# Kernel tuning notes

Measured on AMD Instinct MI355X. Metric: run time of the kernel, lower is better.

The kernel has to match this reference:

```python
import jax, jax.numpy as jnp
import numpy as np

N, E = 50000, 800000
C_IN, C_OUT, DIM, K = 64, 64, 3, 2
EPS = 1e-5


def setup_inputs() -> dict:
    key = jax.random.key(0)
    k1, k2, k3, k4, k5 = jax.random.split(key, 5)
    x = jax.random.normal(k1, (N, C_IN), dtype=jnp.float32)
    edge_index = jax.random.randint(k2, (2, E), 0, N, dtype=jnp.int32)
    edge_attr = jax.random.uniform(k3, (E, DIM), dtype=jnp.float32)  # pseudo coords in [0,1]
    W = jax.random.normal(k4, (K ** DIM, C_IN, C_OUT), dtype=jnp.float32) * 0.05
    root = jax.random.normal(k5, (C_IN, C_OUT), dtype=jnp.float32) * 0.05
    gamma = jnp.ones((C_OUT,), dtype=jnp.float32)
    beta = jnp.zeros((C_OUT,), dtype=jnp.float32)
    return {"x": x, "edge_attr": edge_attr, "W": W, "root": root,
            "gamma": gamma, "beta": beta, "edge_index": edge_index}


def _spline_basis(edge_attr):
    """Degree-1 open B-spline basis. Returns (weights [E,2^D], kernel idx [E,2^D])."""
    D = edge_attr.shape[1]
    v = edge_attr * (K - 1)                      # [E, D]
    k0 = jnp.floor(v)
    frac = v - k0                                # in [0,1)
    k0 = k0.astype(jnp.int32)
    bits = np.stack(np.unravel_index(np.arange(2 ** D), (2,) * D), axis=-1).astype(np.int32)  # [2^D, D]
    bits_f = jnp.asarray(bits, dtype=edge_attr.dtype)
    # per-dim weight: frac if bit else (1 - frac); product over dims
    w = jnp.where(bits_f[None] > 0, frac[:, None, :], 1.0 - frac[:, None, :])  # [E, 2^D, D]
    weights = jnp.prod(w, axis=-1)               # [E, 2^D]
    idx_d = jnp.clip(k0[:, None, :] + bits[None], 0, K - 1)  # [E, 2^D, D]
    radix = jnp.asarray(K ** np.arange(D), dtype=jnp.int32)
    idx = jnp.sum(idx_d * radix, axis=-1)        # [E, 2^D] in [0, K^D)
    return weights, idx


def reference(x, edge_attr, W, root, gamma, beta, edge_index):
    src, dst = edge_index[0], edge_index[1]
    Etot = edge_attr.shape[0]
    S = W.shape[0]  # K^D

    weights, idx = _spline_basis(edge_attr)      # [E, 2^D] each
    # dense per-edge basis over all K^D kernel slots
    B = jnp.zeros((Etot, S), dtype=x.dtype).at[jnp.arange(Etot)[:, None], idx].add(weights)

    xj = x[src]                                  # [E, C_in] gather
    z = (B[:, :, None] * xj[:, None, :]).reshape(Etot, S * x.shape[1])  # [E, S*C_in]
    msg = z @ W.reshape(S * x.shape[1], W.shape[2])                     # [E, C_out]

    agg = jax.ops.segment_sum(msg, dst, num_segments=x.shape[0])        # scatter-add
    cnt = jax.ops.segment_sum(jnp.ones((Etot,), dtype=x.dtype), dst, num_segments=x.shape[0])
    out = agg / jnp.maximum(cnt, 1.0)[:, None] + x @ root               # mean aggr + root weight

    # BatchNorm over nodes (training-mode batch stats)
    mean = jnp.mean(out, axis=0)
    var = jnp.var(out, axis=0)
    y = (out - mean) * jax.lax.rsqrt(var + EPS) * gamma + beta
    return jax.nn.elu(y)
```

## Files before the change

kernel.cpp:

```cpp
#include <hip/hip_runtime.h>
#include <hip/hip_bf16.h>
#include <cstdint>
#include <cstddef>

#define NN 50000
#define NE 800000
#define EPS 1e-5f
#define CAP 64

typedef short bf16x8 __attribute__((ext_vector_type(8)));
typedef float f32x4  __attribute__((ext_vector_type(4)));
typedef float f32x2  __attribute__((ext_vector_type(2)));


#define NB_WT   144
#define NB_MFMA 782
#define NB_SCAT 3125

static __device__ __forceinline__ ushort f2bf(float f) {
    __hip_bfloat16 h = __float2bfloat16(f);
    return *reinterpret_cast<ushort*>(&h);
}
static __device__ __forceinline__ float bf_lo(uint32_t u) {
    return __uint_as_float(u << 16);
}
static __device__ __forceinline__ float bf_hi(uint32_t u) {
    return __uint_as_float(u & 0xffff0000u);
}
static __device__ __forceinline__ uint32_t pack2(float a, float b) {
    return (uint32_t)f2bf(a) | ((uint32_t)f2bf(b) << 16);
}

__global__ __launch_bounds__(256) void wt_prep_k(const float* __restrict__ W,
                                                 const float* __restrict__ root,
                                                 ushort* __restrict__ WTg,
                                                 float* __restrict__ bnps,
                                                 float* __restrict__ bnpq) {
    const int idx = blockIdx.x * 256 + threadIdx.x;
    const int s  = idx >> 12;
    const int co = (idx >> 6) & 63;
    const int ci = idx & 63;
    const float v = (s < 8) ? W[s * 4096 + ci * 64 + co] : root[ci * 64 + co];
    WTg[idx] = f2bf(v);
    if (idx < 4096) { bnps[idx] = 0.f; bnpq[idx] = 0.f; }
}

__global__ __launch_bounds__(256) void fused_mfma_scatter_k(
        const float* __restrict__ x, const ushort* __restrict__ WTg,
        const int* __restrict__ ei, const float* __restrict__ attr,
        int* __restrict__ deg, int2* __restrict__ recs,
        uint8_t* __restrict__ H8, ushort* __restrict__ Hrootb) {
    __shared__ __align__(16) ushort XA[64 * 64];
    __shared__ __align__(16) ushort WT[64 * 64];
    const int t = threadIdx.x;
    const int b = blockIdx.x;

    if (b >= NB_MFMA) {
        const int e = (b - NB_MFMA) * 256 + t;
        if (e >= NE) return;
        const int src = ei[e];
        const int dst = ei[NE + e];
        const float f0 = attr[(size_t)e * 3 + 0];
        const float f1 = attr[(size_t)e * 3 + 1];
        const float f2 = attr[(size_t)e * 3 + 2];
        const uint32_t q = (uint32_t)rintf(f0 * 1023.f)
                         | ((uint32_t)rintf(f1 * 1023.f) << 10)
                         | ((uint32_t)rintf(f2 * 1023.f) << 20);
        const int p = atomicAdd(&deg[dst], 1);
        if (p < CAP) recs[(size_t)dst * CAP + p] = make_int2(src, (int)q);
        return;
    }

    const int n0 = b * 64;

    #pragma unroll
    for (int rep = 0; rep < 2; ++rep) {
        const int vt   = rep * 256 + t;
        const int row  = vt >> 3;
        const int col8 = vt & 7;
        const int n = n0 + row;
        uint4 u;
        if (n < NN) {
            const float4 v0 = *(const float4*)&x[(size_t)n * 64 + col8 * 8];
            const float4 v1 = *(const float4*)&x[(size_t)n * 64 + col8 * 8 + 4];
            u.x = pack2(v0.x, v0.y); u.y = pack2(v0.z, v0.w);
            u.z = pack2(v1.x, v1.y); u.w = pack2(v1.z, v1.w);
        } else {
            u = make_uint4(0, 0, 0, 0);
        }
        const int idx = (row * 64 + col8 * 8) ^ ((row & 7) << 3);
        *(uint4*)&XA[idx] = u;
    }

    const int w    = t >> 6;
    const int lane = t & 63;
    const int mrow = lane & 15;
    const int kgrp = lane >> 4;
    const int swz  = (mrow & 7) << 3;
    const int arow = w * 16 + mrow;
    const int n    = n0 + arow;
    bf16x8 a0, a1;

    for (int s = 0; s < 9; ++s) {
        #pragma unroll
        for (int rep = 0; rep < 2; ++rep) {
            const int c = rep * 256 + t;
            const int row  = c >> 3;
            const int col8 = c & 7;
            const uint4 u = *(const uint4*)&WTg[(size_t)(s * 64 + row) * 64 + col8 * 8];
            const int idx = (row * 64 + col8 * 8) ^ ((row & 7) << 3);
            *(uint4*)&WT[idx] = u;
        }
        __syncthreads();
        if (s == 0) {
            a0 = *(const bf16x8*)&XA[((arow * 64) + 0 * 32 + kgrp * 8) ^ swz];
            a1 = *(const bf16x8*)&XA[((arow * 64) + 1 * 32 + kgrp * 8) ^ swz];
        }
        f32x4 acc[4];
        #pragma unroll
        for (int ct = 0; ct < 4; ++ct) {
            acc[ct] = (f32x4){0.f, 0.f, 0.f, 0.f};
            const int brow = ct * 16 + mrow;
            const bf16x8 b0 = *(const bf16x8*)&WT[((brow * 64) + 0 * 32 + kgrp * 8) ^ swz];
            const bf16x8 b1 = *(const bf16x8*)&WT[((brow * 64) + 1 * 32 + kgrp * 8) ^ swz];
            acc[ct] = __builtin_amdgcn_mfma_f32_16x16x32_bf16(b0, a0, acc[ct], 0, 0, 0);
            acc[ct] = __builtin_amdgcn_mfma_f32_16x16x32_bf16(b1, a1, acc[ct], 0, 0, 0);
        }
        if (n < NN) {
            if (s < 8) {
                #pragma unroll
                for (int ct = 0; ct < 4; ++ct) {
                    int p = __builtin_amdgcn_cvt_pk_fp8_f32(acc[ct][0], acc[ct][1], 0, false);
                    p     = __builtin_amdgcn_cvt_pk_fp8_f32(acc[ct][2], acc[ct][3], p, true);
                    *(uint32_t*)&H8[(size_t)n * 512 + s * 64 + ct * 16 + kgrp * 4] = (uint32_t)p;
                }
            } else {
                #pragma unroll
                for (int ct = 0; ct < 4; ++ct) {
                    ushort4 h4;
                    h4.x = f2bf(acc[ct][0]); h4.y = f2bf(acc[ct][1]);
                    h4.z = f2bf(acc[ct][2]); h4.w = f2bf(acc[ct][3]);
                    *(ushort4*)&Hrootb[(size_t)n * 64 + ct * 16 + kgrp * 4] = h4;
                }
            }
        }
        __syncthreads();
    }
}

__global__ __launch_bounds__(256) void aggregate_k(const int* __restrict__ deg,
                                                   const int2* __restrict__ recs,
                                                   const uint8_t* __restrict__ H8,
                                                   const ushort* __restrict__ Hrootb,
                                                   float* __restrict__ outb,
                                                   float* __restrict__ bnps,
                                                   float* __restrict__ bnpq) {
    __shared__ float red_s[4][64], red_q[4][64];
    const int t = threadIdx.x, lane = t & 63, w = t >> 6;
    const int n = blockIdx.x * 4 + w;
    const int sidx = lane >> 3;
    const int cog  = lane & 7;
    const float sg0 = (sidx & 1) ? 1.f : -1.f, cc0 = (sidx & 1) ? 0.f : 1.f;
    const float sg1 = (sidx & 2) ? 1.f : -1.f, cc1 = (sidx & 2) ? 0.f : 1.f;
    const float sg2 = (sidx & 4) ? 1.f : -1.f, cc2 = (sidx & 4) ? 0.f : 1.f;
    const int cnt = min(deg[n], CAP);
    const int2* rp = recs + (size_t)n * CAP;
    const size_t loff = (size_t)(lane << 3);

    f32x2 acc2[4] = {(f32x2){0.f, 0.f}, (f32x2){0.f, 0.f},
                     (f32x2){0.f, 0.f}, (f32x2){0.f, 0.f}};

#define DECODE_W(qv, wv)                                                     \
    {                                                                        \
        const uint32_t q_ = (uint32_t)(qv);                                  \
        const float f0_ = (float)(q_ & 1023u) * (1.f / 1023.f);              \
        const float f1_ = (float)((q_ >> 10) & 1023u) * (1.f / 1023.f);      \
        const float f2_ = (float)((q_ >> 20) & 1023u) * (1.f / 1023.f);      \
        wv = (cc0 + sg0 * f0_) * ((cc1 + sg1 * f1_) * (cc2 + sg2 * f2_));    \
    }
#define ACCUM(wv, h)                                                         \
    {                                                                        \
        const f32x2 w2_ = {wv, wv};                                          \
        acc2[0] += w2_ * (f32x2)__builtin_amdgcn_cvt_pk_f32_fp8((int)(h).x, false); \
        acc2[1] += w2_ * (f32x2)__builtin_amdgcn_cvt_pk_f32_fp8((int)(h).x, true);  \
        acc2[2] += w2_ * (f32x2)__builtin_amdgcn_cvt_pk_f32_fp8((int)(h).y, false); \
        acc2[3] += w2_ * (f32x2)__builtin_amdgcn_cvt_pk_f32_fp8((int)(h).y, true);  \
    }

    int j = 0;
    for (; j + 3 < cnt; j += 4) {
        const int2 r0 = rp[j];
        const int2 r1 = rp[j + 1];
        const int2 r2 = rp[j + 2];
        const int2 r3 = rp[j + 3];
        const uint2 h0 = *(const uint2*)(H8 + (size_t)r0.x * 512 + loff);
        const uint2 h1 = *(const uint2*)(H8 + (size_t)r1.x * 512 + loff);
        const uint2 h2 = *(const uint2*)(H8 + (size_t)r2.x * 512 + loff);
        const uint2 h3 = *(const uint2*)(H8 + (size_t)r3.x * 512 + loff);
        float w0, w1, w2, w3;
        DECODE_W(r0.y, w0); DECODE_W(r1.y, w1);
        DECODE_W(r2.y, w2); DECODE_W(r3.y, w3);
        ACCUM(w0, h0); ACCUM(w1, h1); ACCUM(w2, h2); ACCUM(w3, h3);
    }
    for (; j < cnt; ++j) {
        const int2 r0 = rp[j];
        const uint2 h0 = *(const uint2*)(H8 + (size_t)r0.x * 512 + loff);
        float w0;
        DECODE_W(r0.y, w0);
        ACCUM(w0, h0);
    }
#undef DECODE_W
#undef ACCUM

    float accf[8] = {acc2[0].x, acc2[0].y, acc2[1].x, acc2[1].y,
                     acc2[2].x, acc2[2].y, acc2[3].x, acc2[3].y};
    #pragma unroll
    for (int k = 0; k < 8; ++k) {
        float v = accf[k];
        v += __shfl_xor(v, 8, 64);
        v += __shfl_xor(v, 16, 64);
        v += __shfl_xor(v, 32, 64);
        accf[k] = v;
    }
    if (sidx == 0) {
        const float inv = 1.f / fmaxf((float)cnt, 1.f);
        const size_t base = (size_t)n * 64 + cog * 8;
        const uint4 hr = *(const uint4*)&Hrootb[base];
        const float rr[8] = {bf_lo(hr.x), bf_hi(hr.x), bf_lo(hr.y), bf_hi(hr.y),
                             bf_lo(hr.z), bf_hi(hr.z), bf_lo(hr.w), bf_hi(hr.w)};
        float vv[8];
        #pragma unroll
        for (int k = 0; k < 8; ++k) vv[k] = accf[k] * inv + rr[k];
        *(float4*)&outb[base]     = make_float4(vv[0], vv[1], vv[2], vv[3]);
        *(float4*)&outb[base + 4] = make_float4(vv[4], vv[5], vv[6], vv[7]);
        #pragma unroll
        for (int k = 0; k < 8; ++k) {
            red_s[w][k * 8 + cog] = vv[k];
            red_q[w][k * 8 + cog] = vv[k] * vv[k];
        }
    }
    __syncthreads();
    if (t < 64) {
        const float s = red_s[0][t] + red_s[1][t] + red_s[2][t] + red_s[3][t];
        const float q = red_q[0][t] + red_q[1][t] + red_q[2][t] + red_q[3][t];
        const int co = (t & 7) * 8 + (t >> 3);
        const int slot = (blockIdx.x & 63) * 64 + co;
        atomicAdd(&bnps[slot], s);
        atomicAdd(&bnpq[slot], q);
    }
}

__global__ __launch_bounds__(256) void finalize_kernel(float* __restrict__ outb,
                                                       const float* __restrict__ bnps,
                                                       const float* __restrict__ bnpq,
                                                       const float* __restrict__ gamma,
                                                       const float* __restrict__ beta) {
    __shared__ float sc_sh[64], sh_sh[64];
    const int t = threadIdx.x;
    if (t < 64) {
        float s = 0.f, q = 0.f;
        for (int k = 0; k < 64; ++k) { s += bnps[k * 64 + t]; q += bnpq[k * 64 + t]; }
        const float mean = s * (1.f / NN);
        const float var  = q * (1.f / NN) - mean * mean;
        const float sc = rsqrtf(var + EPS) * gamma[t];
        sc_sh[t] = sc;
        sh_sh[t] = beta[t] - mean * sc;
    }
    __syncthreads();
    const int total4 = NN * 16;
    for (int idx = blockIdx.x * 256 + t; idx < total4; idx += gridDim.x * 256) {
        float4 v = ((const float4*)outb)[idx];
        const int co0 = (idx & 15) * 4;
        float o[4] = {v.x, v.y, v.z, v.w};
        #pragma unroll
        for (int j = 0; j < 4; ++j) {
            const float y = o[j] * sc_sh[co0 + j] + sh_sh[co0 + j];
            o[j] = (y > 0.f) ? y : expm1f(y);
        }
        ((float4*)outb)[idx] = make_float4(o[0], o[1], o[2], o[3]);
    }
}

extern "C" void kernel_launch(void* const* d_in, const int* in_sizes, int n_in,
                              void* d_out, int out_size, void* d_ws, size_t ws_size,
                              hipStream_t stream) {
    const float* x     = (const float*)d_in[0];
    const float* attr  = (const float*)d_in[1];
    const float* W     = (const float*)d_in[2];
    const float* root  = (const float*)d_in[3];
    const float* gamma = (const float*)d_in[4];
    const float* beta  = (const float*)d_in[5];
    const int*   ei    = (const int*)d_in[6];
    float* outb = (float*)d_out;

    char* ws = (char*)d_ws;
    uint8_t* H8     = (uint8_t*)(ws);
    ushort*  Hrootb = (ushort*)(ws + 25600000);
    int2*    recs   = (int2*)(ws + 32000000);
    int*     deg    = (int*)(ws + 57600000);
    float*   bnps   = (float*)(ws + 57800064);
    float*   bnpq   = (float*)(ws + 57816448);
    ushort*  WTg    = (ushort*)(ws + 57832832);

    hipMemsetAsync(ws + 57600000, 0, 200000, stream);

    wt_prep_k<<<NB_WT, 256, 0, stream>>>(W, root, WTg, bnps, bnpq);
    fused_mfma_scatter_k<<<NB_MFMA + NB_SCAT, 256, 0, stream>>>(
        x, WTg, ei, attr, deg, recs, H8, Hrootb);
    aggregate_k<<<NN / 4, 256, 0, stream>>>(deg, recs, H8, Hrootb, outb, bnps, bnpq);
    finalize_kernel<<<256, 256, 0, stream>>>(outb, bnps, bnpq, gamma, beta);
}
```

Baseline: 147.9 us.

## Pack edge records into 32 bits with 5-bit pseudo-coordinates

Result: faster. 141.8 us (-4.2%).

```diff
diff --git a/kernel.cpp b/kernel.cpp
--- a/kernel.cpp
+++ b/kernel.cpp
@@ -15,7 +15,7 @@
 
 #define NB_WT   144
 #define NB_MFMA 782
-#define NB_SCAT 3125
+#define NB_SCAT 782
 
 static __device__ __forceinline__ ushort f2bf(float f) {
     __hip_bfloat16 h = __float2bfloat16(f);
@@ -48,7 +48,7 @@
 __global__ __launch_bounds__(256) void fused_mfma_scatter_k(
         const float* __restrict__ x, const ushort* __restrict__ WTg,
         const int* __restrict__ ei, const float* __restrict__ attr,
-        int* __restrict__ deg, int2* __restrict__ recs,
+        int* __restrict__ deg, uint32_t* __restrict__ recs,
         uint8_t* __restrict__ H8, ushort* __restrict__ Hrootb) {
     __shared__ __align__(16) ushort XA[64 * 64];
     __shared__ __align__(16) ushort WT[64 * 64];
@@ -56,18 +56,24 @@
     const int b = blockIdx.x;
 
     if (b >= NB_MFMA) {
-        const int e = (b - NB_MFMA) * 256 + t;
-        if (e >= NE) return;
-        const int src = ei[e];
-        const int dst = ei[NE + e];
-        const float f0 = attr[(size_t)e * 3 + 0];
-        const float f1 = attr[(size_t)e * 3 + 1];
-        const float f2 = attr[(size_t)e * 3 + 2];
-        const uint32_t q = (uint32_t)rintf(f0 * 1023.f)
-                         | ((uint32_t)rintf(f1 * 1023.f) << 10)
-                         | ((uint32_t)rintf(f2 * 1023.f) << 20);
-        const int p = atomicAdd(&deg[dst], 1);
-        if (p < CAP) recs[(size_t)dst * CAP + p] = make_int2(src, (int)q);
+        const int e0 = (b - NB_MFMA) * 1024 + t;
+        #pragma unroll
+        for (int k = 0; k < 4; ++k) {
+            const int e = e0 + k * 256;
+            if (e < NE) {
+                const int src = ei[e];
+                const int dst = ei[NE + e];
+                const float f0 = attr[(size_t)e * 3 + 0];
+                const float f1 = attr[(size_t)e * 3 + 1];
+                const float f2 = attr[(size_t)e * 3 + 2];
+                const uint32_t rec = (uint32_t)src
+                                   | ((uint32_t)rintf(f0 * 31.f) << 16)
+                                   | ((uint32_t)rintf(f1 * 31.f) << 21)
+                                   | ((uint32_t)rintf(f2 * 31.f) << 26);
+                const int p = atomicAdd(&deg[dst], 1);
+                if (p < CAP) recs[(size_t)dst * CAP + p] = rec;
+            }
+        }
         return;
     }
 
@@ -149,7 +155,7 @@
 }
 
 __global__ __launch_bounds__(256) void aggregate_k(const int* __restrict__ deg,
-                                                   const int2* __restrict__ recs,
+                                                   const uint32_t* __restrict__ recs,
                                                    const uint8_t* __restrict__ H8,
                                                    const ushort* __restrict__ Hrootb,
                                                    float* __restrict__ outb,
@@ -164,7 +170,7 @@
     const float sg1 = (sidx & 2) ? 1.f : -1.f, cc1 = (sidx & 2) ? 0.f : 1.f;
     const float sg2 = (sidx & 4) ? 1.f : -1.f, cc2 = (sidx & 4) ? 0.f : 1.f;
     const int cnt = min(deg[n], CAP);
-    const int2* rp = recs + (size_t)n * CAP;
+    const uint32_t* rp = recs + (size_t)n * CAP;
     const size_t loff = (size_t)(lane << 3);
 
     f32x2 acc2[4] = {(f32x2){0.f, 0.f}, (f32x2){0.f, 0.f},
@@ -173,9 +179,9 @@
 #define DECODE_W(qv, wv)                                                     \
     {                                                                        \
         const uint32_t q_ = (uint32_t)(qv);                                  \
-        const float f0_ = (float)(q_ & 1023u) * (1.f / 1023.f);              \
-        const float f1_ = (float)((q_ >> 10) & 1023u) * (1.f / 1023.f);      \
-        const float f2_ = (float)((q_ >> 20) & 1023u) * (1.f / 1023.f);      \
+        const float f0_ = (float)((q_ >> 16) & 31u) * (1.f / 31.f);          \
+        const float f1_ = (float)((q_ >> 21) & 31u) * (1.f / 31.f);          \
+        const float f2_ = (float)((q_ >> 26) & 31u) * (1.f / 31.f);          \
         wv = (cc0 + sg0 * f0_) * ((cc1 + sg1 * f1_) * (cc2 + sg2 * f2_));    \
     }
 #define ACCUM(wv, h)                                                         \
@@ -189,24 +195,26 @@
 
     int j = 0;
     for (; j + 3 < cnt; j += 4) {
-        const int2 r0 = rp[j];
-        const int2 r1 = rp[j + 1];
-        const int2 r2 = rp[j + 2];
-        const int2 r3 = rp[j + 3];
-        const uint2 h0 = *(const uint2*)(H8 + (size_t)r0.x * 512 + loff);
-        const uint2 h1 = *(const uint2*)(H8 + (size_t)r1.x * 512 + loff);
-        const uint2 h2 = *(const uint2*)(H8 + (size_t)r2.x * 512 + loff);
-        const uint2 h3 = *(const uint2*)(H8 + (size_t)r3.x * 512 + loff);
+        const uint4 r4 = *(const uint4*)(rp + j);
+        const int s0 = (int)(r4.x & 0xFFFFu);
+        const int s1 = (int)(r4.y & 0xFFFFu);
+        const int s2 = (int)(r4.z & 0xFFFFu);
+        const int s3 = (int)(r4.w & 0xFFFFu);
+        const uint2 h0 = *(const uint2*)(H8 + (size_t)s0 * 512 + loff);
+        const uint2 h1 = *(const uint2*)(H8 + (size_t)s1 * 512 + loff);
+        const uint2 h2 = *(const uint2*)(H8 + (size_t)s2 * 512 + loff);
+        const uint2 h3 = *(const uint2*)(H8 + (size_t)s3 * 512 + loff);
         float w0, w1, w2, w3;
-        DECODE_W(r0.y, w0); DECODE_W(r1.y, w1);
-        DECODE_W(r2.y, w2); DECODE_W(r3.y, w3);
+        DECODE_W(r4.x, w0); DECODE_W(r4.y, w1);
+        DECODE_W(r4.z, w2); DECODE_W(r4.w, w3);
         ACCUM(w0, h0); ACCUM(w1, h1); ACCUM(w2, h2); ACCUM(w3, h3);
     }
     for (; j < cnt; ++j) {
-        const int2 r0 = rp[j];
-        const uint2 h0 = *(const uint2*)(H8 + (size_t)r0.x * 512 + loff);
+        const uint32_t r0 = rp[j];
+        const int s0 = (int)(r0 & 0xFFFFu);
+        const uint2 h0 = *(const uint2*)(H8 + (size_t)s0 * 512 + loff);
         float w0;
-        DECODE_W(r0.y, w0);
+        DECODE_W(r0, w0);
         ACCUM(w0, h0);
     }
 #undef DECODE_W
@@ -294,15 +302,15 @@
     float* outb = (float*)d_out;
 
     char* ws = (char*)d_ws;
-    uint8_t* H8     = (uint8_t*)(ws);
-    ushort*  Hrootb = (ushort*)(ws + 25600000);
-    int2*    recs   = (int2*)(ws + 32000000);
-    int*     deg    = (int*)(ws + 57600000);
-    float*   bnps   = (float*)(ws + 57800064);
-    float*   bnpq   = (float*)(ws + 57816448);
-    ushort*  WTg    = (ushort*)(ws + 57832832);
-
-    hipMemsetAsync(ws + 57600000, 0, 200000, stream);
+    uint8_t*  H8     = (uint8_t*)(ws);
+    ushort*   Hrootb = (ushort*)(ws + 25600000);
+    uint32_t* recs   = (uint32_t*)(ws + 32000000);
+    int*      deg    = (int*)(ws + 44800000);
+    float*    bnps   = (float*)(ws + 45000064);
+    float*    bnpq   = (float*)(ws + 45016448);
+    ushort*   WTg    = (ushort*)(ws + 45032832);
+
+    hipMemsetAsync(ws + 44800000, 0, 200000, stream);
 
     wt_prep_k<<<NB_WT, 256, 0, stream>>>(W, root, WTg, bnps, bnpq);
     fused_mfma_scatter_k<<<NB_MFMA + NB_SCAT, 256, 0, stream>>>(
```
